# Kernel tuning notes

Measured on AMD Instinct MI355X. Metric: run time of the kernel, lower is better.

## Reference

```python
import jax, jax.numpy as jnp
import numpy as np

# dims
H = 1024          # hidden_size
E = 2048          # d_inner = 2*H
NH = 32           # nheads = E/64
P = 64            # headdim
N = 128           # d_state
G = 1             # ngroups
K = 4             # d_conv
Q = 128           # SSD chunk length
FF = 4096         # intermediate_size
EPS = 1e-6        # rms_norm_eps
NEPS = 1e-5       # mamba gated-norm eps
CONV_DIM = E + 2 * G * N            # 2304
D_IN = 2 * E + 2 * G * N + NH       # 4384


def rmsnorm(x, w, eps):
    v = jnp.mean(x.astype(jnp.float32) ** 2, axis=-1, keepdims=True)
    return (x.astype(jnp.float32) * jax.lax.rsqrt(v + eps)).astype(x.dtype) * w


def segsum(x):
    # x: [..., T] -> [..., T, T] with out[i,j] = sum_{j<k<=i} x[k], -inf above diag
    T = x.shape[-1]
    cs = jnp.cumsum(x, axis=-1)
    s = cs[..., :, None] - cs[..., None, :]
    mask = jnp.tril(jnp.ones((T, T), dtype=bool))
    return jnp.where(mask, s, -jnp.inf)


def ssd(x, dt, A_log, B, C):
    # x:[b,l,nh,p], dt:[b,l,nh], B,C:[b,l,N] (ngroups=1, shared over heads)
    b, l, nh, p = x.shape
    A = -jnp.exp(A_log)                      # [nh]
    dA = dt * A                              # [b,l,nh]
    xd = x * dt[..., None]                   # discretized input
    c = l // Q
    xd = xd.reshape(b, c, Q, nh, p)
    dAc = dA.reshape(b, c, Q, nh).transpose(0, 3, 1, 2)   # [b,h,c,q]
    Bc = B.reshape(b, c, Q, N)
    Cc = C.reshape(b, c, Q, N)
    A_cs = jnp.cumsum(dAc, axis=-1)                        # [b,h,c,q]
    Lm = jnp.exp(segsum(dAc))                              # [b,h,c,q,q]
    # intra-chunk (diagonal blocks)
    Y_diag = jnp.einsum('bcqn,bcsn,bhcqs,bcshp->bcqhp', Cc, Bc, Lm, xd)
    # per-chunk final states
    decay_states = jnp.exp(A_cs[..., -1:] - A_cs)          # [b,h,c,q]
    states = jnp.einsum('bcqn,bhcq,bcqhp->bchpn', Bc, decay_states, xd)
    # inter-chunk recurrence (initial state = 0)
    A_last = jnp.pad(A_cs[..., -1], ((0, 0), (0, 0), (1, 0)))   # [b,h,c+1]
    decay_chunk = jnp.exp(segsum(A_last))                       # [b,h,c+1,c+1]
    states = jnp.concatenate([jnp.zeros_like(states[:, :1]), states], axis=1)
    new_states = jnp.einsum('bhzc,bchpn->bzhpn', decay_chunk, states)[:, :-1]
    Y_off = jnp.einsum('bcqn,bchpn,bhcq->bcqhp', Cc, new_states, jnp.exp(A_cs))
    return (Y_diag + Y_off).reshape(b, l, nh, p)


def mamba2(h, w_in, w_conv, b_conv, dt_bias, A_log, D, w_mnorm, w_out):
    b, l, _ = h.shape
    zxbcdt = h @ w_in.T                         # [b,l,D_IN]
    z, xBC, dt = jnp.split(zxbcdt, [E, E + CONV_DIM], axis=-1)
    # causal depthwise conv (kernel K) over channels of xBC
    pad = jnp.pad(xBC, ((0, 0), (K - 1, 0), (0, 0)))
    xBC = sum(pad[:, k:k + l, :] * w_conv[:, k] for k in range(K)) + b_conv
    xBC = jax.nn.silu(xBC)
    x, B, C = jnp.split(xBC, [E, E + G * N], axis=-1)
    dt = jax.nn.softplus(dt + dt_bias)          # [b,l,NH]
    xh = x.reshape(b, l, NH, P)
    y = ssd(xh, dt, A_log, B, C)
    y = y + D[None, None, :, None] * xh         # per-head skip
    y = y.reshape(b, l, E)
    y = rmsnorm(y * jax.nn.silu(z), w_mnorm, NEPS)   # gated RMSNorm
    return y @ w_out.T


def setup_inputs() -> dict:
    key = jax.random.key(0)
    ks = jax.random.split(key, 12)
    dt0 = jax.random.uniform(ks[0], (NH,), minval=0.001, maxval=0.1)
    dt_bias = dt0 + jnp.log(-jnp.expm1(-dt0))   # inverse softplus
    return {
        'hidden_states': jax.random.normal(ks[1], (2, 2048, H), dtype=jnp.float32),
        'w_ln1': jnp.ones((H,), jnp.float32),
        'w_in': 0.02 * jax.random.normal(ks[2], (D_IN, H), dtype=jnp.float32),
        'w_conv': 0.1 * jax.random.normal(ks[3], (CONV_DIM, K), dtype=jnp.float32),
        'b_conv': jnp.zeros((CONV_DIM,), jnp.float32),
        'dt_bias': dt_bias,
        'A_log': jnp.log(jax.random.uniform(ks[4], (NH,), minval=1.0, maxval=16.0)),
        'D': jnp.ones((NH,), jnp.float32),
        'w_mnorm': jnp.ones((E,), jnp.float32),
        'w_out': 0.02 * jax.random.normal(ks[5], (H, E), dtype=jnp.float32),
        'w_ln2': jnp.ones((H,), jnp.float32),
        'w_gate': 0.02 * jax.random.normal(ks[6], (FF, H), dtype=jnp.float32),
        'w_up': 0.02 * jax.random.normal(ks[7], (FF, H), dtype=jnp.float32),
        'w_down': 0.02 * jax.random.normal(ks[8], (H, FF), dtype=jnp.float32),
    }


def reference(hidden_states, w_ln1, w_in, w_conv, b_conv, dt_bias, A_log, D,
              w_mnorm, w_out, w_ln2, w_gate, w_up, w_down):
    residual = hidden_states
    h = rmsnorm(hidden_states, w_ln1, EPS)
    h = mamba2(h, w_in, w_conv, b_conv, dt_bias, A_log, D, w_mnorm, w_out)
    hidden = residual + h
    residual = hidden
    h = rmsnorm(hidden, w_ln2, EPS)
    h = (jax.nn.silu(h @ w_gate.T) * (h @ w_up.T)) @ w_down.T
    return residual + h
```

## Files before the change

kernel.cpp:

```cpp
#include <hip/hip_runtime.h>

#define DEV static __device__ __forceinline__

typedef short bf16x8 __attribute__((ext_vector_type(8)));
typedef float floatx4 __attribute__((ext_vector_type(4)));
typedef unsigned short ushort4v __attribute__((ext_vector_type(4)));
typedef unsigned short ushort8v __attribute__((ext_vector_type(8)));

DEV unsigned short f32_bf16(float f) {
  unsigned int u = __builtin_bit_cast(unsigned int, f);
  u = u + 0x7fffu + ((u >> 16) & 1u);
  return (unsigned short)(u >> 16);
}
DEV float bf2f(unsigned short u) {
  unsigned int v = ((unsigned int)u) << 16;
  return __builtin_bit_cast(float, v);
}
DEV float sigmoidf_(float x) { return 1.0f / (1.0f + __expf(-x)); }
DEV float siluf_(float x) { return x * sigmoidf_(x); }

#define GLD_LDS16(g, l)                                                              \
  __builtin_amdgcn_global_load_lds((const __attribute__((address_space(1))) void*)(g), \
                                   (__attribute__((address_space(3))) void*)(l), 16, 0, 0)

template <int MODE, int BN>
__global__ __launch_bounds__(256) void gemm128(
    const unsigned short* __restrict__ A, const unsigned short* __restrict__ B,
    void* __restrict__ Cv, const unsigned short* __restrict__ other,
    int K, int lda, int ldb, int ldc, long long bsA, long long bsB, long long bsC) {
  constexpr int NBG = BN / 64;
  constexpr int NJ = BN / 32;
  constexpr int BUFSZ = 4096 + BN * 32;
  __shared__ unsigned short S[2 * BUFSZ];
  A += (long long)blockIdx.z * bsA;
  B += (long long)blockIdx.z * bsB;
  const long long coff = (long long)blockIdx.z * bsC;
  const int tid = threadIdx.x;
  const int w = tid >> 6, lane = tid & 63;

  const int nbx = gridDim.x, nby = gridDim.y;
  const int GM = 4;
  int bid = blockIdx.y * nbx + blockIdx.x;
  int gid = bid / (GM * nbx);
  int rem = bid - gid * (GM * nbx);
  int gsz = min(GM, nby - gid * GM);
  int mtile = gid * GM + rem % gsz;
  int ntile = rem / gsz;
  const int m0 = mtile << 7, n0 = ntile * BN;

  const int srow = lane >> 2;
  const int schunk = ((lane & 3) ^ (srow & 3)) * 8;
  const unsigned short* ag0 = A + (long long)(m0 + w * 32 + srow) * lda + schunk;
  const unsigned short* ag1 = ag0 + (long long)16 * lda;
  const unsigned short* bgp[NBG];
#pragma unroll
  for (int ii = 0; ii < NBG; ++ii)
    bgp[ii] = B + (long long)(n0 + w * (BN / 4) + srow + 16 * ii) * ldb + schunk;

  auto STAGE = [&](int buf, int k0) {
    unsigned short* as_ = S + buf * BUFSZ;
    unsigned short* bs_ = as_ + 4096;
    GLD_LDS16(ag0 + k0, as_ + w * 1024 + lane * 8);
    GLD_LDS16(ag1 + k0, as_ + w * 1024 + lane * 8 + 512);
#pragma unroll
    for (int ii = 0; ii < NBG; ++ii)
      GLD_LDS16(bgp[ii] + k0, bs_ + w * (NBG * 512) + ii * 512 + lane * 8);
  };

  const int wr = (w >> 1) << 6;
  const int wc = (w & 1) * (BN / 2);
  const int fr = lane & 15;
  const int slot = (((lane >> 4) ^ (fr & 3))) << 3;
  const int r0 = (lane >> 4) << 2;

  floatx4 acc[4][NJ];
#pragma unroll
  for (int i = 0; i < 4; ++i)
#pragma unroll
    for (int j = 0; j < NJ; ++j) acc[i][j] = (floatx4){0.f, 0.f, 0.f, 0.f};

  const int nsteps = K >> 5;
  STAGE(0, 0);
  if (nsteps > 1) STAGE(1, 32);

  for (int t = 0; t < nsteps; ++t) {
    if (t < nsteps - 1) {
      if constexpr (NBG == 2) {
        asm volatile("s_waitcnt vmcnt(4)" ::: "memory");
      } else {
        asm volatile("s_waitcnt vmcnt(6)" ::: "memory");
      }
    } else {
      asm volatile("s_waitcnt vmcnt(0)" ::: "memory");
    }
    __builtin_amdgcn_s_barrier();
    __builtin_amdgcn_sched_barrier(0);
    const unsigned short* Ab = S + (t & 1) * BUFSZ;
    const unsigned short* Bb = Ab + 4096;
    bf16x8 af[4], bf_[NJ];
#pragma unroll
    for (int i = 0; i < 4; ++i)
      af[i] = *(const bf16x8*)(Ab + (wr + i * 16 + fr) * 32 + slot);
#pragma unroll
    for (int j = 0; j < NJ; ++j)
      bf_[j] = *(const bf16x8*)(Bb + (wc + j * 16 + fr) * 32 + slot);
#pragma unroll
    for (int i = 0; i < 4; ++i)
#pragma unroll
      for (int j = 0; j < NJ; ++j)
        acc[i][j] = __builtin_amdgcn_mfma_f32_16x16x32_bf16(af[i], bf_[j], acc[i][j], 0, 0, 0);
    __builtin_amdgcn_sched_barrier(0);
    __builtin_amdgcn_s_barrier();
    if (t + 2 < nsteps) STAGE(t & 1, (t + 2) * 32);
  }

  if constexpr (MODE == 0) {
#pragma unroll
    for (int i = 0; i < 4; ++i) {
#pragma unroll
      for (int j = 0; j < NJ; ++j) {
        long long base = (long long)(m0 + wr + i * 16 + r0) * ldc + (n0 + wc + j * 16 + fr);
#pragma unroll
        for (int r = 0; r < 4; ++r) {
          ((float*)Cv)[coff + base + (long long)r * ldc] = acc[i][j][r];
        }
      }
    }
  } else {
    constexpr int PAD = BN + 4;
    float* scr = (float*)S;
    const int row_l = tid >> 3;
    const int col0 = (tid & 7) * 8;
    __syncthreads();
#pragma unroll
    for (int pass = 0; pass < 4; ++pass) {
      if ((w >> 1) == (pass >> 1)) {
#pragma unroll
        for (int ii = 0; ii < 2; ++ii) {
          int i = (pass & 1) * 2 + ii;
          int rl = i * 16 + r0 - (pass & 1) * 32;
#pragma unroll
          for (int j = 0; j < NJ; ++j) {
            int col = wc + j * 16 + fr;
#pragma unroll
            for (int r = 0; r < 4; ++r) scr[(rl + r) * PAD + col] = acc[i][j][r];
          }
        }
      }
      __syncthreads();
      long long grow = m0 + pass * 32 + row_l;
      long long gbase = coff + grow * ldc + n0;
      const float* srow_p = scr + row_l * PAD;
#pragma unroll
      for (int k = 0; k < BN / 64; ++k) {
        int col = col0 + k * 64;
        float v[8];
        *(float4*)&v[0] = *(const float4*)(srow_p + col);
        *(float4*)&v[4] = *(const float4*)(srow_p + col + 4);
        ushort8v o;
        if constexpr (MODE == 2) {
          ushort8v uo = *(const ushort8v*)(other + gbase + col);
#pragma unroll
          for (int e = 0; e < 8; ++e) o[e] = f32_bf16(siluf_(v[e]) * bf2f(uo[e]));
        } else {
#pragma unroll
          for (int e = 0; e < 8; ++e) o[e] = f32_bf16(v[e]);
        }
        *(ushort8v*)((unsigned short*)Cv + gbase + col) = o;
      }
      __syncthreads();
    }
  }
}

template <int WM>
__global__ __launch_bounds__(256) void gemm_small_nt(
    const unsigned short* __restrict__ A, const unsigned short* __restrict__ B,
    float* __restrict__ C, int M, int N, int K, int lda, int ldb, int ldc) {
  const int w = threadIdx.x >> 6;
  const int lane = threadIdx.x & 63;
  const int lm = lane & 15;
  const int ko = (lane >> 4) << 3;
  const int bn0 = blockIdx.x << 6;
  const int m_base = blockIdx.y * (WM * 64) + w * (WM * 16);

  const unsigned short* arow[WM];
#pragma unroll
  for (int i = 0; i < WM; ++i) arow[i] = A + (long long)(m_base + i * 16 + lm) * lda + ko;
  int nv = (N - bn0) >> 4;
  nv = nv > 4 ? 4 : nv;
  const unsigned short* brow[4];
#pragma unroll
  for (int j = 0; j < 4; ++j) {
    int nr = bn0 + j * 16 + lm;
    brow[j] = B + (long long)(j < nv ? nr : 0) * ldb + ko;
  }
  floatx4 acc[WM][4];
#pragma unroll
  for (int i = 0; i < WM; ++i)
#pragma unroll
    for (int j = 0; j < 4; ++j) acc[i][j] = (floatx4){0.f, 0.f, 0.f, 0.f};
  for (int k0 = 0; k0 < K; k0 += 32) {
    bf16x8 a[WM];
#pragma unroll
    for (int i = 0; i < WM; ++i) a[i] = *(const bf16x8*)(arow[i] + k0);
#pragma unroll
    for (int j = 0; j < 4; ++j) {
      if (j < nv) {
        bf16x8 b = *(const bf16x8*)(brow[j] + k0);
#pragma unroll
        for (int i = 0; i < WM; ++i)
          acc[i][j] = __builtin_amdgcn_mfma_f32_16x16x32_bf16(a[i], b, acc[i][j], 0, 0, 0);
      }
    }
  }
  const int r0 = (lane >> 4) << 2;
#pragma unroll
  for (int i = 0; i < WM; ++i)
#pragma unroll
    for (int j = 0; j < 4; ++j)
      if (j < nv) {
        int col = bn0 + j * 16 + lm;
        long long base = (long long)(m_base + i * 16 + r0) * ldc + col;
#pragma unroll
        for (int r = 0; r < 4; ++r) C[base + (long long)r * ldc] = acc[i][j][r];
      }
}

__global__ __launch_bounds__(256) void wconv_all_k(
    const float* __restrict__ w_in, const float* __restrict__ w_gate,
    const float* __restrict__ w_up, const float* __restrict__ w_down,
    const float* __restrict__ w_out, unsigned short* __restrict__ d_in_,
    unsigned short* __restrict__ d_gate, unsigned short* __restrict__ d_up,
    unsigned short* __restrict__ d_down, unsigned short* __restrict__ d_out_) {
  long long j = (long long)blockIdx.x * 256 + threadIdx.x;
  const float* src;
  unsigned short* dst;
  if (j < 1122304) {
    src = w_in; dst = d_in_;
  } else if ((j -= 1122304) < 1048576) {
    src = w_gate; dst = d_gate;
  } else if ((j -= 1048576) < 1048576) {
    src = w_up; dst = d_up;
  } else if ((j -= 1048576) < 1048576) {
    src = w_down; dst = d_down;
  } else if ((j -= 1048576) < 524288) {
    src = w_out; dst = d_out_;
  } else {
    return;
  }
  float4 v = ((const float4*)src)[j];
  ushort4v o = {f32_bf16(v.x), f32_bf16(v.y), f32_bf16(v.z), f32_bf16(v.w)};
  ((ushort4v*)dst)[j] = o;
}

__global__ __launch_bounds__(256) void zero_out_k(float* __restrict__ o, long long n) {
  long long i = (long long)blockIdx.x * 256 + threadIdx.x;
  if (i < n) o[i] = 0.f;
}

__global__ __launch_bounds__(256) void rmsnorm1024_bf16_k(const float* __restrict__ x,
                                                          const float* __restrict__ w,
                                                          unsigned short* __restrict__ out,
                                                          float eps) {
  long long row = blockIdx.x;
  int t = threadIdx.x;
  float4 v = ((const float4*)(x + row * 1024))[t];
  float ss = v.x * v.x + v.y * v.y + v.z * v.z + v.w * v.w;
  __shared__ float red[4];
#pragma unroll
  for (int o = 32; o > 0; o >>= 1) ss += __shfl_down(ss, o, 64);
  if ((t & 63) == 0) red[t >> 6] = ss;
  __syncthreads();
  float tot = red[0] + red[1] + red[2] + red[3];
  float sc = rsqrtf(tot * (1.0f / 1024.0f) + eps);
  float4 wv = ((const float4*)w)[t];
  ushort4v o = {f32_bf16(v.x * sc * wv.x), f32_bf16(v.y * sc * wv.y),
                f32_bf16(v.z * sc * wv.z), f32_bf16(v.w * sc * wv.w)};
  ((ushort4v*)(out + row * 1024))[t] = o;
}

__global__ __launch_bounds__(256) void add_rmsnorm_k(const float* __restrict__ hs,
                                                     const float* __restrict__ parts,
                                                     long long pstride, int np,
                                                     const float* __restrict__ w,
                                                     float* __restrict__ mh,
                                                     unsigned short* __restrict__ h2, float eps) {
  long long row = blockIdx.x;
  int t = threadIdx.x;
  float4 v = ((const float4*)(hs + row * 1024))[t];
  for (int p = 0; p < np; ++p) {
    float4 u = ((const float4*)(parts + p * pstride + row * 1024))[t];
    v.x += u.x;
    v.y += u.y;
    v.z += u.z;
    v.w += u.w;
  }
  ((float4*)(mh + row * 1024))[t] = v;
  float ss = v.x * v.x + v.y * v.y + v.z * v.z + v.w * v.w;
  __shared__ float red[4];
#pragma unroll
  for (int o = 32; o > 0; o >>= 1) ss += __shfl_down(ss, o, 64);
  if ((t & 63) == 0) red[t >> 6] = ss;
  __syncthreads();
  float tot = red[0] + red[1] + red[2] + red[3];
  float sc = rsqrtf(tot * (1.0f / 1024.0f) + eps);
  float4 wv = ((const float4*)w)[t];
  ushort4v o = {f32_bf16(v.x * sc * wv.x), f32_bf16(v.y * sc * wv.y),
                f32_bf16(v.z * sc * wv.z), f32_bf16(v.w * sc * wv.w)};
  ((ushort4v*)(h2 + row * 1024))[t] = o;
}

__global__ __launch_bounds__(256) void addn_f32_k(const float* __restrict__ a,
                                                  const float* __restrict__ parts,
                                                  long long pstride, int np,
                                                  float* __restrict__ o, long long n4) {
  long long i = (long long)blockIdx.x * 256 + threadIdx.x;
  if (i < n4) {
    float4 x = ((const float4*)a)[i];
    for (int p = 0; p < np; ++p) {
      float4 u = ((const float4*)(parts + p * pstride))[i];
      x.x += u.x;
      x.y += u.y;
      x.z += u.z;
      x.w += u.w;
    }
    ((float4*)o)[i] = x;
  }
}

__global__ __launch_bounds__(256) void gated_rmsnorm2048_k(const unsigned short* __restrict__ y,
                                                           const unsigned short* __restrict__ z,
                                                           const float* __restrict__ w,
                                                           unsigned short* __restrict__ out,
                                                           float eps) {
  long long row = blockIdx.x;
  int t = threadIdx.x;
  ushort8v yv = ((const ushort8v*)(y + row * 2048))[t];
  ushort8v zv = ((const ushort8v*)(z + row * 2048))[t];
  float g[8];
  float ss = 0.f;
#pragma unroll
  for (int j = 0; j < 8; ++j) {
    g[j] = bf2f(yv[j]) * siluf_(bf2f(zv[j]));
    ss += g[j] * g[j];
  }
  __shared__ float red[4];
#pragma unroll
  for (int o = 32; o > 0; o >>= 1) ss += __shfl_down(ss, o, 64);
  if ((t & 63) == 0) red[t >> 6] = ss;
  __syncthreads();
  float tot = red[0] + red[1] + red[2] + red[3];
  float sc = rsqrtf(tot * (1.0f / 2048.0f) + eps);
  float ww[8];
  *(float4*)&ww[0] = ((const float4*)w)[2 * t];
  *(float4*)&ww[4] = ((const float4*)w)[2 * t + 1];
  ushort8v o;
#pragma unroll
  for (int j = 0; j < 8; ++j) o[j] = f32_bf16(g[j] * sc * ww[j]);
  ((ushort8v*)(out + row * 2048))[t] = o;
}

__global__ __launch_bounds__(256) void conv_silu_k(const unsigned short* __restrict__ xraw,
                                                   const float* __restrict__ wconv,
                                                   const float* __restrict__ bconv,
                                                   unsigned short* __restrict__ xBC) {
  long long f = (long long)blockIdx.x * 256 + threadIdx.x;
  if (f >= 4096LL * 288) return;
  int m = (int)(f / 288);
  int cb = (int)(f - (long long)m * 288);
  int l = m & 2047;
  int ch0 = cb << 3;
  float acc[8];
  float4 bc0 = ((const float4*)bconv)[cb * 2];
  float4 bc1 = ((const float4*)bconv)[cb * 2 + 1];
  acc[0] = bc0.x; acc[1] = bc0.y; acc[2] = bc0.z; acc[3] = bc0.w;
  acc[4] = bc1.x; acc[5] = bc1.y; acc[6] = bc1.z; acc[7] = bc1.w;
  float4 wv[8];
#pragma unroll
  for (int j = 0; j < 8; ++j) wv[j] = ((const float4*)wconv)[ch0 + j];
#pragma unroll
  for (int k = 0; k < 4; ++k) {
    int lk = l + k - 3;
    if (lk >= 0) {
      ushort8v xv = *(const ushort8v*)(xraw + (long long)(m + k - 3) * 2304 + ch0);
      acc[0] += bf2f(xv[0]) * ((const float*)&wv[0])[k];
      acc[1] += bf2f(xv[1]) * ((const float*)&wv[1])[k];
      acc[2] += bf2f(xv[2]) * ((const float*)&wv[2])[k];
      acc[3] += bf2f(xv[3]) * ((const float*)&wv[3])[k];
      acc[4] += bf2f(xv[4]) * ((const float*)&wv[4])[k];
      acc[5] += bf2f(xv[5]) * ((const float*)&wv[5])[k];
      acc[6] += bf2f(xv[6]) * ((const float*)&wv[6])[k];
      acc[7] += bf2f(xv[7]) * ((const float*)&wv[7])[k];
    }
  }
  ushort8v o;
#pragma unroll
  for (int j = 0; j < 8; ++j) o[j] = f32_bf16(siluf_(acc[j]));
  *(ushort8v*)(xBC + (long long)m * 2304 + ch0) = o;
}

__global__ __launch_bounds__(128) void dA_cumsum_k(const float* __restrict__ dtraw,
                                                   const float* __restrict__ dt_bias,
                                                   const float* __restrict__ A_log,
                                                   float* __restrict__ dt_s,
                                                   float* __restrict__ dA_cs) {
  int bi = blockIdx.x;
  int c = bi & 15, h = (bi >> 4) & 31, b = bi >> 9;
  int q = threadIdx.x;
  long long idx = ((long long)(b * 2048 + c * 128 + q)) * 32 + h;
  float xv = dtraw[idx] + dt_bias[h];
  float sp = xv > 20.f ? xv : log1pf(expf(xv));
  dt_s[idx] = sp;
  float A = -expf(A_log[h]);
  float v = sp * A;
  __shared__ float sbuf[128];
  sbuf[q] = v;
  __syncthreads();
  for (int off = 1; off < 128; off <<= 1) {
    float tv = (q >= off) ? sbuf[q - off] : 0.f;
    __syncthreads();
    sbuf[q] += tv;
    __syncthreads();
  }
  dA_cs[(long long)bi * 128 + q] = sbuf[q];
}

__global__ __launch_bounds__(256) void ssd_diag_states_k(
    const unsigned short* __restrict__ xBC, const float* __restrict__ dt_s,
    const float* __restrict__ dA_cs, const unsigned short* __restrict__ G,
    unsigned short* __restrict__ y, unsigned short* __restrict__ states) {
  __shared__ unsigned short Mz[128 * 136];
  __shared__ unsigned short xdT[64 * 136];
  __shared__ float Acs[128];
  __shared__ float wdec[128];
  const int bx = blockIdx.x;
  const int h = bx & 31, c = (bx >> 5) & 15, b = bx >> 9;
  const int t = threadIdx.x;
  const int w = t >> 6, lane = t & 63, fr = lane & 15, hi = lane >> 4;
  const long long rowbase = (long long)b * 2048 + c * 128;
  const long long abase = ((long long)((b * 32 + h) * 16 + c)) << 7;

  if (t < 128) {
    float a = dA_cs[abase + t];
    Acs[t] = a;
    wdec[t] = __expf(dA_cs[abase + 127] - a);
  }
  {
    int s = t >> 1, p0 = (t & 1) * 32;
    float dtv = dt_s[(rowbase + s) * 32 + h];
    const ushort8v* xv = (const ushort8v*)(xBC + (rowbase + s) * 2304 + h * 64 + p0);
#pragma unroll
    for (int i = 0; i < 4; ++i) {
      ushort8v vv = xv[i];
#pragma unroll
      for (int j = 0; j < 8; ++j) xdT[(p0 + i * 8 + j) * 136 + s] = f32_bf16(bf2f(vv[j]) * dtv);
    }
  }
  __syncthreads();
  {
    int q = t >> 1, s0 = (t & 1) * 64;
    float aq = Acs[q];
    const ushort8v* gv =
        (const ushort8v*)(G + (((long long)(b * 16 + c)) * 128 + q) * 128 + s0);
#pragma unroll
    for (int i = 0; i < 8; ++i) {
      ushort8v gg = gv[i];
      ushort8v mo;
#pragma unroll
      for (int j = 0; j < 8; ++j) {
        int s = s0 + i * 8 + j;
        float m = (s <= q) ? bf2f(gg[j]) * __expf(aq - Acs[s]) : 0.f;
        mo[j] = f32_bf16(m);
      }
      *(ushort8v*)(Mz + q * 136 + s0 + i * 8) = mo;
    }
  }
  __syncthreads();
  const int q0 = w << 5;
  {
    floatx4 acc[2][4];
#pragma unroll
    for (int i = 0; i < 2; ++i)
#pragma unroll
      for (int j = 0; j < 4; ++j) acc[i][j] = (floatx4){0.f, 0.f, 0.f, 0.f};
#pragma unroll
    for (int k0 = 0; k0 < 128; k0 += 32) {
      int kk = k0 + hi * 8;
      bf16x8 a0 = *(const bf16x8*)(Mz + (q0 + fr) * 136 + kk);
      bf16x8 a1 = *(const bf16x8*)(Mz + (q0 + 16 + fr) * 136 + kk);
      bf16x8 bf_[4];
#pragma unroll
      for (int j = 0; j < 4; ++j) bf_[j] = *(const bf16x8*)(xdT + (j * 16 + fr) * 136 + kk);
#pragma unroll
      for (int j = 0; j < 4; ++j) {
        acc[0][j] = __builtin_amdgcn_mfma_f32_16x16x32_bf16(a0, bf_[j], acc[0][j], 0, 0, 0);
        acc[1][j] = __builtin_amdgcn_mfma_f32_16x16x32_bf16(a1, bf_[j], acc[1][j], 0, 0, 0);
      }
    }
    __syncthreads();
    float* scr = (float*)Mz;
#pragma unroll
    for (int i = 0; i < 2; ++i)
#pragma unroll
      for (int r = 0; r < 4; ++r) {
        int q = q0 + i * 16 + hi * 4 + r;
#pragma unroll
        for (int j = 0; j < 4; ++j) scr[q * 68 + j * 16 + fr] = acc[i][j][r];
      }
    __syncthreads();
    {
      int row = t >> 1, colh = (t & 1) * 32;
      unsigned short* yrow = y + (rowbase + row) * 2048 + h * 64 + colh;
      const float* sp = scr + row * 68 + colh;
#pragma unroll
      for (int k = 0; k < 4; ++k) {
        float4 v0 = *(const float4*)(sp + k * 8);
        float4 v1 = *(const float4*)(sp + k * 8 + 4);
        ushort8v o = {f32_bf16(v0.x), f32_bf16(v0.y), f32_bf16(v0.z), f32_bf16(v0.w),
                      f32_bf16(v1.x), f32_bf16(v1.y), f32_bf16(v1.z), f32_bf16(v1.w)};
        *(ushort8v*)(yrow + k * 8) = o;
      }
    }
  }
  __syncthreads();
  {
    int s = t >> 1, n0 = (t & 1) * 64;
    float wd = wdec[s];
    const ushort8v* bv = (const ushort8v*)(xBC + (rowbase + s) * 2304 + 2048 + n0);
#pragma unroll
    for (int i = 0; i < 8; ++i) {
      ushort8v bb = bv[i];
#pragma unroll
      for (int j = 0; j < 8; ++j) Mz[(n0 + i * 8 + j) * 136 + s] = f32_bf16(bf2f(bb[j]) * wd);
    }
  }
  __syncthreads();
  {
    floatx4 acc[2][4];
#pragma unroll
    for (int i = 0; i < 2; ++i)
#pragma unroll
      for (int j = 0; j < 4; ++j) acc[i][j] = (floatx4){0.f, 0.f, 0.f, 0.f};
#pragma unroll
    for (int k0 = 0; k0 < 128; k0 += 32) {
      int kk = k0 + hi * 8;
      bf16x8 a0 = *(const bf16x8*)(Mz + (q0 + fr) * 136 + kk);
      bf16x8 a1 = *(const bf16x8*)(Mz + (q0 + 16 + fr) * 136 + kk);
      bf16x8 bf_[4];
#pragma unroll
      for (int j = 0; j < 4; ++j) bf_[j] = *(const bf16x8*)(xdT + (j * 16 + fr) * 136 + kk);
#pragma unroll
      for (int j = 0; j < 4; ++j) {
        acc[0][j] = __builtin_amdgcn_mfma_f32_16x16x32_bf16(a0, bf_[j], acc[0][j], 0, 0, 0);
        acc[1][j] = __builtin_amdgcn_mfma_f32_16x16x32_bf16(a1, bf_[j], acc[1][j], 0, 0, 0);
      }
    }
    __syncthreads();
    float* scr = (float*)Mz;
#pragma unroll
    for (int i = 0; i < 2; ++i)
#pragma unroll
      for (int j = 0; j < 4; ++j) {
        int p = j * 16 + fr;
        int n = q0 + i * 16 + hi * 4;
#pragma unroll
        for (int r = 0; r < 4; ++r) scr[p * 132 + n + r] = acc[i][j][r];
      }
    __syncthreads();
    {
      unsigned short* st = states + (long long)bx * 8192;
      int p = t >> 2, nh = (t & 3) * 32;
      unsigned short* strow = st + p * 128 + nh;
      const float* sp = scr + p * 132 + nh;
#pragma unroll
      for (int k = 0; k < 4; ++k) {
        float4 v0 = *(const float4*)(sp + k * 8);
        float4 v1 = *(const float4*)(sp + k * 8 + 4);
        ushort8v o = {f32_bf16(v0.x), f32_bf16(v0.y), f32_bf16(v0.z), f32_bf16(v0.w),
                      f32_bf16(v1.x), f32_bf16(v1.y), f32_bf16(v1.z), f32_bf16(v1.w)};
        *(ushort8v*)(strow + k * 8) = o;
      }
    }
  }
}

__global__ __launch_bounds__(256) void ssd_scan_k(const float* __restrict__ dA_cs,
                                                  unsigned short* __restrict__ states) {
  int seg = blockIdx.x & 3;
  int h = (blockIdx.x >> 2) & 31;
  int b = blockIdx.x >> 7;
  int t = threadIdx.x;
  int e0 = seg * 2048 + t * 8;
  float carry[8];
#pragma unroll
  for (int i = 0; i < 8; ++i) carry[i] = 0.f;
  for (int c = 0; c < 16; ++c) {
    long long base = ((long long)((b * 16 + c) * 32 + h)) * 8192;
    float dec = __expf(dA_cs[(((long long)((b * 32 + h) * 16 + c)) << 7) + 127]);
    ushort8v v = *(const ushort8v*)(states + base + e0);
    ushort8v o;
#pragma unroll
    for (int i = 0; i < 8; ++i) {
      float local = bf2f(v[i]);
      o[i] = f32_bf16(carry[i]);
      carry[i] = dec * carry[i] + local;
    }
    *(ushort8v*)(states + base + e0) = o;
  }
}

__global__ __launch_bounds__(256) void ssd_off_k(const unsigned short* __restrict__ xBC,
                                                 const float* __restrict__ dA_cs,
                                                 const unsigned short* __restrict__ states,
                                                 const float* __restrict__ Dvec,
                                                 unsigned short* __restrict__ y) {
  __shared__ float eA[128];
  __shared__ float scr[128 * 68];
  const int bx = blockIdx.x;
  const int h = bx & 31, c = (bx >> 5) & 15, b = bx >> 9;
  const int t = threadIdx.x;
  const int w = t >> 6, lane = t & 63, fr = lane & 15, hi = lane >> 4;
  const long long rowbase = (long long)b * 2048 + c * 128;
  const long long abase = ((long long)((b * 32 + h) * 16 + c)) << 7;
  if (t < 128) eA[t] = __expf(dA_cs[abase + t]);
  __syncthreads();

  const unsigned short* st = states + (long long)bx * 8192;
  const int q0 = w << 5;
  floatx4 acc[2][4];
#pragma unroll
  for (int i = 0; i < 2; ++i)
#pragma unroll
    for (int j = 0; j < 4; ++j) acc[i][j] = (floatx4){0.f, 0.f, 0.f, 0.f};

#pragma unroll
  for (int k0 = 0; k0 < 128; k0 += 32) {
    int kk = k0 + hi * 8;
    bf16x8 a0 = *(const bf16x8*)(xBC + (rowbase + q0 + fr) * 2304 + 2176 + kk);
    bf16x8 a1 = *(const bf16x8*)(xBC + (rowbase + q0 + 16 + fr) * 2304 + 2176 + kk);
    bf16x8 bf_[4];
#pragma unroll
    for (int j = 0; j < 4; ++j) bf_[j] = *(const bf16x8*)(st + (j * 16 + fr) * 128 + kk);
#pragma unroll
    for (int j = 0; j < 4; ++j) {
      acc[0][j] = __builtin_amdgcn_mfma_f32_16x16x32_bf16(a0, bf_[j], acc[0][j], 0, 0, 0);
      acc[1][j] = __builtin_amdgcn_mfma_f32_16x16x32_bf16(a1, bf_[j], acc[1][j], 0, 0, 0);
    }
  }

#pragma unroll
  for (int i = 0; i < 2; ++i)
#pragma unroll
    for (int r = 0; r < 4; ++r) {
      int q = q0 + i * 16 + hi * 4 + r;
#pragma unroll
      for (int j = 0; j < 4; ++j) scr[q * 68 + j * 16 + fr] = acc[i][j][r];
    }
  __syncthreads();
  {
    float Dh = Dvec[h];
    int row = t >> 1, colh = (t & 1) * 32;
    float e = eA[row];
    const unsigned short* xrow = xBC + (rowbase + row) * 2304 + h * 64 + colh;
    unsigned short* yrow = y + (rowbase + row) * 2048 + h * 64 + colh;
    const float* sp = scr + row * 68 + colh;
#pragma unroll
    for (int k = 0; k < 4; ++k) {
      ushort8v yv = *(const ushort8v*)(yrow + k * 8);
      ushort8v xv = *(const ushort8v*)(xrow + k * 8);
      float4 a0 = *(const float4*)(sp + k * 8);
      float4 a1 = *(const float4*)(sp + k * 8 + 4);
      float av[8] = {a0.x, a0.y, a0.z, a0.w, a1.x, a1.y, a1.z, a1.w};
      ushort8v o;
#pragma unroll
      for (int e2 = 0; e2 < 8; ++e2)
        o[e2] = f32_bf16(bf2f(yv[e2]) + e * av[e2] + Dh * bf2f(xv[e2]));
      *(ushort8v*)(yrow + k * 8) = o;
    }
  }
}

extern "C" void kernel_launch(void* const* d_in, const int* in_sizes, int n_in, void* d_out,
                              int out_size, void* d_ws, size_t ws_size, hipStream_t stream) {
  const float* hs = (const float*)d_in[0];
  const float* w_ln1 = (const float*)d_in[1];
  const float* w_in = (const float*)d_in[2];
  const float* w_conv = (const float*)d_in[3];
  const float* b_conv = (const float*)d_in[4];
  const float* dt_bias = (const float*)d_in[5];
  const float* A_log = (const float*)d_in[6];
  const float* Dvec = (const float*)d_in[7];
  const float* w_mnorm = (const float*)d_in[8];
  const float* w_out = (const float*)d_in[9];
  const float* w_ln2 = (const float*)d_in[10];
  const float* w_gate = (const float*)d_in[11];
  const float* w_up = (const float*)d_in[12];
  const float* w_down = (const float*)d_in[13];
  float* out = (float*)d_out;
  const int M = 4096;

  char* ws = (char*)d_ws;
  const size_t R0 = 0;
  const size_t R1 = 33554432;
  const size_t R1b = R1 + 33554432;
  const size_t R2 = 71303168;
  const size_t R3 = 90177536;
  const size_t R4 = 107544576;
  const size_t W0 = 108068864;
  const size_t NEED = 133234688;

  if (ws_size < NEED) {
    hipLaunchKernelGGL(zero_out_k, dim3((out_size + 255) / 256), dim3(256), 0, stream, out,
                       (long long)out_size);
    return;
  }

  unsigned short* z = (unsigned short*)(ws + R0);
  unsigned short* act = (unsigned short*)(ws + R0);
  float* oproj_parts = (float*)(ws + R0);
  unsigned short* xraw = (unsigned short*)(ws + R1);
  unsigned short* states = (unsigned short*)(ws + R1);
  unsigned short* ybuf = (unsigned short*)(ws + R1 + 16777216);
  unsigned short* upo = (unsigned short*)(ws + R1);
  float* down_parts = (float*)(ws + R1);
  unsigned short* wbf_out = (unsigned short*)(ws + R1b);
  unsigned short* xBC = (unsigned short*)(ws + R2);
  unsigned short* ygn = (unsigned short*)(ws + R2);
  unsigned short* h2 = (unsigned short*)(ws + R2);
  unsigned short* hnorm = (unsigned short*)(ws + R3);
  unsigned short* wbf_in = (unsigned short*)(ws + R3 + 8388608);
  float* dt_s = (float*)(ws + R3);
  float* dA_cs = (float*)(ws + R3 + 524288);
  unsigned short* Gbuf = (unsigned short*)(ws + R3 + 1048576);
  float* mh = (float*)(ws + R3);
  float* dtraw = (float*)(ws + R4);
  unsigned short* wbf_gate = (unsigned short*)(ws + W0);
  unsigned short* wbf_up = (unsigned short*)(ws + W0 + 8388608);
  unsigned short* wbf_down = (unsigned short*)(ws + W0 + 16777216);

  hipLaunchKernelGGL(rmsnorm1024_bf16_k, dim3(M), dim3(256), 0, stream, hs, w_ln1, hnorm, 1e-6f);
  hipLaunchKernelGGL(wconv_all_k, dim3(18720), dim3(256), 0, stream, w_in, w_gate, w_up, w_down,
                     w_out, wbf_in, wbf_gate, wbf_up, wbf_down, wbf_out);
  hipLaunchKernelGGL((gemm128<1, 128>), dim3(16, 32, 1), dim3(256), 0, stream, hnorm, wbf_in,
                     (void*)z, (const unsigned short*)nullptr, 1024, 1024, 1024, 2048, 0LL, 0LL,
                     0LL);
  hipLaunchKernelGGL((gemm128<1, 128>), dim3(18, 32, 1), dim3(256), 0, stream, hnorm,
                     wbf_in + 2048 * 1024, (void*)xraw, (const unsigned short*)nullptr, 1024, 1024,
                     1024, 2304, 0LL, 0LL, 0LL);
  hipLaunchKernelGGL((gemm_small_nt<1>), dim3(1, 64, 1), dim3(256), 0, stream, hnorm,
                     wbf_in + 4352 * 1024, dtraw, M, 32, 1024, 1024, 1024, 32);
  hipLaunchKernelGGL(conv_silu_k, dim3(4608), dim3(256), 0, stream, xraw, w_conv, b_conv, xBC);
  hipLaunchKernelGGL(dA_cumsum_k, dim3(1024), dim3(128), 0, stream, dtraw, dt_bias, A_log, dt_s,
                     dA_cs);
  hipLaunchKernelGGL((gemm128<1, 128>), dim3(1, 1, 32), dim3(256), 0, stream, xBC + 2176,
                     xBC + 2048, (void*)Gbuf, (const unsigned short*)nullptr, 128, 2304, 2304, 128,
                     294912LL, 294912LL, 16384LL);
  hipLaunchKernelGGL(ssd_diag_states_k, dim3(1024), dim3(256), 0, stream, xBC, dt_s, dA_cs, Gbuf,
                     ybuf, states);
  hipLaunchKernelGGL(ssd_scan_k, dim3(256), dim3(256), 0, stream, dA_cs, states);
  hipLaunchKernelGGL(ssd_off_k, dim3(1024), dim3(256), 0, stream, xBC, dA_cs, states, Dvec, ybuf);
  hipLaunchKernelGGL(gated_rmsnorm2048_k, dim3(M), dim3(256), 0, stream, ybuf, z, w_mnorm, ygn,
                     1e-5f);
  hipLaunchKernelGGL((gemm128<0, 128>), dim3(8, 32, 2), dim3(256), 0, stream, ygn, wbf_out,
                     (void*)oproj_parts, (const unsigned short*)nullptr, 1024, 2048, 2048, 1024,
                     1024LL, 1024LL, 4194304LL);
  hipLaunchKernelGGL(add_rmsnorm_k, dim3(M), dim3(256), 0, stream, hs, oproj_parts, 4194304LL, 2,
                     w_ln2, mh, h2, 1e-6f);
  hipLaunchKernelGGL((gemm128<1, 256>), dim3(16, 32, 1), dim3(256), 0, stream, h2, wbf_up,
                     (void*)upo, (const unsigned short*)nullptr, 1024, 1024, 1024, 4096, 0LL, 0LL,
                     0LL);
  hipLaunchKernelGGL((gemm128<2, 256>), dim3(16, 32, 1), dim3(256), 0, stream, h2, wbf_gate,
                     (void*)act, upo, 1024, 1024, 1024, 4096, 0LL, 0LL, 0LL);
  hipLaunchKernelGGL((gemm128<0, 128>), dim3(8, 32, 2), dim3(256), 0, stream, act, wbf_down,
                     (void*)down_parts, (const unsigned short*)nullptr, 2048, 4096, 4096, 1024,
                     2048LL, 2048LL, 4194304LL);
  hipLaunchKernelGGL(addn_f32_k, dim3(4096), dim3(256), 0, stream, mh, down_parts, 4194304LL, 2,
                     out, 1048576LL);
}
```

Before: 523.3 us.

## Fuse gate and up projections into a dual-B GEMM with SiLU epilogue

Replaces the two separate up and gate GEMM launches with one kernel that loads the shared A tile once and accumulates both gate and up products on 128x128 tiles, then applies silu(gate)*up in registers before writing bf16. This removes the intermediate up-projection write and read and halves the A-tile loads, and it adds grouped tile ordering for L2 reuse. In exchange it doubles accumulator registers per thread (two 4x4 floatx4 sets), which may force lower occupancy or spills, and it uses smaller N tiles than the previous 256-wide variant.

After: 511.9 us. 2.2% less time.

```diff
diff --git a/kernel.cpp b/kernel.cpp
--- a/kernel.cpp
+++ b/kernel.cpp
@@ -170,6 +170,141 @@
       }
       __syncthreads();
     }
+  }
+}
+
+__global__ __launch_bounds__(256, 2) void gemm128_dual(
+    const unsigned short* __restrict__ A, const unsigned short* __restrict__ Bg,
+    const unsigned short* __restrict__ Bu, unsigned short* __restrict__ C,
+    int K, int lda, int ldb, int ldc) {
+  __shared__ unsigned short S[2 * 12288];
+  const int tid = threadIdx.x;
+  const int w = tid >> 6, lane = tid & 63;
+  const int nbx = gridDim.x, nby = gridDim.y;
+  const int GM = 4;
+  int bid = blockIdx.y * nbx + blockIdx.x;
+  int gid = bid / (GM * nbx);
+  int rem = bid - gid * (GM * nbx);
+  int gsz = min(GM, nby - gid * GM);
+  int mtile = gid * GM + rem % gsz;
+  int ntile = rem / gsz;
+  const int m0 = mtile << 7, n0 = ntile << 7;
+
+  const int srow = lane >> 2;
+  const int schunk = ((lane & 3) ^ (srow & 3)) * 8;
+  const unsigned short* ag0 = A + (long long)(m0 + w * 32 + srow) * lda + schunk;
+  const unsigned short* ag1 = ag0 + (long long)16 * lda;
+  const unsigned short* gg0 = Bg + (long long)(n0 + w * 32 + srow) * ldb + schunk;
+  const unsigned short* gg1 = gg0 + (long long)16 * ldb;
+  const unsigned short* ug0 = Bu + (long long)(n0 + w * 32 + srow) * ldb + schunk;
+  const unsigned short* ug1 = ug0 + (long long)16 * ldb;
+
+  auto STAGE = [&](int buf, int k0) {
+    unsigned short* as_ = S + buf * 12288;
+    unsigned short* gs_ = as_ + 4096;
+    unsigned short* us_ = as_ + 8192;
+    GLD_LDS16(ag0 + k0, as_ + w * 1024 + lane * 8);
+    GLD_LDS16(ag1 + k0, as_ + w * 1024 + lane * 8 + 512);
+    GLD_LDS16(gg0 + k0, gs_ + w * 1024 + lane * 8);
+    GLD_LDS16(gg1 + k0, gs_ + w * 1024 + lane * 8 + 512);
+    GLD_LDS16(ug0 + k0, us_ + w * 1024 + lane * 8);
+    GLD_LDS16(ug1 + k0, us_ + w * 1024 + lane * 8 + 512);
+  };
+
+  const int wr = (w >> 1) << 6;
+  const int wc = (w & 1) << 6;
+  const int fr = lane & 15;
+  const int slot = (((lane >> 4) ^ (fr & 3))) << 3;
+  const int r0 = (lane >> 4) << 2;
+
+  floatx4 accg[4][4], accu[4][4];
+#pragma unroll
+  for (int i = 0; i < 4; ++i)
+#pragma unroll
+    for (int j = 0; j < 4; ++j) {
+      accg[i][j] = (floatx4){0.f, 0.f, 0.f, 0.f};
+      accu[i][j] = (floatx4){0.f, 0.f, 0.f, 0.f};
+    }
+
+  const int nsteps = K >> 5;
+  STAGE(0, 0);
+  if (nsteps > 1) STAGE(1, 32);
+
+  for (int t = 0; t < nsteps; ++t) {
+    if (t < nsteps - 1) {
+      asm volatile("s_waitcnt vmcnt(6)" ::: "memory");
+    } else {
+      asm volatile("s_waitcnt vmcnt(0)" ::: "memory");
+    }
+    __builtin_amdgcn_s_barrier();
+    __builtin_amdgcn_sched_barrier(0);
+    const unsigned short* Ab = S + (t & 1) * 12288;
+    const unsigned short* Gb = Ab + 4096;
+    const unsigned short* Ub = Ab + 8192;
+    bf16x8 af[4], gf[4], uf[4];
+#pragma unroll
+    for (int i = 0; i < 4; ++i)
+      af[i] = *(const bf16x8*)(Ab + (wr + i * 16 + fr) * 32 + slot);
+#pragma unroll
+    for (int j = 0; j < 4; ++j) {
+      gf[j] = *(const bf16x8*)(Gb + (wc + j * 16 + fr) * 32 + slot);
+      uf[j] = *(const bf16x8*)(Ub + (wc + j * 16 + fr) * 32 + slot);
+    }
+#pragma unroll
+    for (int i = 0; i < 4; ++i)
+#pragma unroll
+      for (int j = 0; j < 4; ++j) {
+        accg[i][j] = __builtin_amdgcn_mfma_f32_16x16x32_bf16(af[i], gf[j], accg[i][j], 0, 0, 0);
+        accu[i][j] = __builtin_amdgcn_mfma_f32_16x16x32_bf16(af[i], uf[j], accu[i][j], 0, 0, 0);
+      }
+    __builtin_amdgcn_sched_barrier(0);
+    __builtin_amdgcn_s_barrier();
+    if (t + 2 < nsteps) STAGE(t & 1, (t + 2) * 32);
+  }
+
+#pragma unroll
+  for (int i = 0; i < 4; ++i)
+#pragma unroll
+    for (int j = 0; j < 4; ++j)
+#pragma unroll
+      for (int r = 0; r < 4; ++r) accg[i][j][r] = siluf_(accg[i][j][r]) * accu[i][j][r];
+
+  constexpr int PAD = 132;
+  float* scr = (float*)S;
+  const int row_l = tid >> 3;
+  const int col0 = (tid & 7) * 8;
+  __syncthreads();
+#pragma unroll
+  for (int pass = 0; pass < 4; ++pass) {
+    if ((w >> 1) == (pass >> 1)) {
+#pragma unroll
+      for (int ii = 0; ii < 2; ++ii) {
+        int i = (pass & 1) * 2 + ii;
+        int rl = i * 16 + r0 - (pass & 1) * 32;
+#pragma unroll
+        for (int j = 0; j < 4; ++j) {
+          int col = wc + j * 16 + fr;
+#pragma unroll
+          for (int r = 0; r < 4; ++r) scr[(rl + r) * PAD + col] = accg[i][j][r];
+        }
+      }
+    }
+    __syncthreads();
+    long long grow = m0 + pass * 32 + row_l;
+    long long gbase = grow * (long long)ldc + n0;
+    const float* srow_p = scr + row_l * PAD;
+#pragma unroll
+    for (int k = 0; k < 2; ++k) {
+      int col = col0 + k * 64;
+      float v[8];
+      *(float4*)&v[0] = *(const float4*)(srow_p + col);
+      *(float4*)&v[4] = *(const float4*)(srow_p + col + 4);
+      ushort8v o;
+#pragma unroll
+      for (int e = 0; e < 8; ++e) o[e] = f32_bf16(v[e]);
+      *(ushort8v*)(C + gbase + col) = o;
+    }
+    __syncthreads();
   }
 }
 
@@ -722,7 +857,6 @@
   unsigned short* xraw = (unsigned short*)(ws + R1);
   unsigned short* states = (unsigned short*)(ws + R1);
   unsigned short* ybuf = (unsigned short*)(ws + R1 + 16777216);
-  unsigned short* upo = (unsigned short*)(ws + R1);
   float* down_parts = (float*)(ws + R1);
   unsigned short* wbf_out = (unsigned short*)(ws + R1b);
   unsigned short* xBC = (unsigned short*)(ws + R2);
@@ -767,11 +901,8 @@
                      1024LL, 1024LL, 4194304LL);
   hipLaunchKernelGGL(add_rmsnorm_k, dim3(M), dim3(256), 0, stream, hs, oproj_parts, 4194304LL, 2,
                      w_ln2, mh, h2, 1e-6f);
-  hipLaunchKernelGGL((gemm128<1, 256>), dim3(16, 32, 1), dim3(256), 0, stream, h2, wbf_up,
-                     (void*)upo, (const unsigned short*)nullptr, 1024, 1024, 1024, 4096, 0LL, 0LL,
-                     0LL);
-  hipLaunchKernelGGL((gemm128<2, 256>), dim3(16, 32, 1), dim3(256), 0, stream, h2, wbf_gate,
-                     (void*)act, upo, 1024, 1024, 1024, 4096, 0LL, 0LL, 0LL);
+  hipLaunchKernelGGL(gemm128_dual, dim3(32, 32, 1), dim3(256), 0, stream, h2, wbf_gate, wbf_up,
+                     act, 1024, 1024, 1024, 4096);
   hipLaunchKernelGGL((gemm128<0, 128>), dim3(8, 32, 2), dim3(256), 0, stream, act, wbf_down,
                      (void*)down_parts, (const unsigned short*)nullptr, 2048, 4096, 4096, 1024,
                      2048LL, 2048LL, 4194304LL);
```
